# Performance work log

Hardware: AMD Instinct MI355X
Metric: run time of the kernel (lower is better)

The kernel has to match this reference:

```python
import jax, jax.numpy as jnp
import numpy as np
from jax import lax

C = 64; H = 128; W = 256; HW = H * W
HIDDEN = 64
D_STATE = 64; HEADDIM = 64; EXPAND = 2; CHUNK = 256; CONV_K = 4
D_INNER = EXPAND * C            # 128
NHEADS = D_INNER // HEADDIM     # 2
CONV_DIM = D_INNER + 2 * D_STATE  # 256
D_IN_PROJ = 2 * D_INNER + 2 * D_STATE + NHEADS  # 386
RECORD_LEN = [5, 3, 4, 2]
EPS = 1e-5


def setup_inputs() -> dict:
    key = jax.random.key(0)
    ks = jax.random.split(key, 16)
    def nrm(k, shape, scale=0.02):
        return scale * jax.random.normal(k, shape, jnp.float32)
    return {
        "xx": jax.random.normal(ks[0], (sum(RECORD_LEN), C, H, W), jnp.float32),
        "record_len": jnp.array(RECORD_LEN, jnp.int32),
        "score_w1": nrm(ks[1], (HIDDEN, C)),
        "score_b1": jnp.zeros((HIDDEN,), jnp.float32),
        "score_w2": nrm(ks[2], (1, HIDDEN)),
        "score_b2": jnp.zeros((1,), jnp.float32),
        "q_w": nrm(ks[3], (C, C)), "q_b": jnp.zeros((C,), jnp.float32),
        "k_w": nrm(ks[4], (C, C)), "k_b": jnp.zeros((C,), jnp.float32),
        "v_w": nrm(ks[5], (C, C)), "v_b": jnp.zeros((C,), jnp.float32),
        "ln_w": jnp.ones((C,), jnp.float32), "ln_b": jnp.zeros((C,), jnp.float32),
        "in_proj_w": nrm(ks[6], (D_IN_PROJ, C)),
        "in_proj_b": jnp.zeros((D_IN_PROJ,), jnp.float32),
        "conv_w": nrm(ks[7], (CONV_DIM, 1, CONV_K), 0.1),
        "conv_b": jnp.zeros((CONV_DIM,), jnp.float32),
        "dt_bias": 0.1 * jax.random.normal(ks[8], (NHEADS,), jnp.float32),
        "A_log": jnp.log(jnp.arange(1, NHEADS + 1, dtype=jnp.float32)),
        "ssd_D": jnp.ones((NHEADS,), jnp.float32),
        "rms_w": jnp.ones((D_INNER,), jnp.float32),
        "out_proj_w": nrm(ks[9], (C, D_INNER)),
    }


def _segsum(x):
    # x: (..., T) -> (..., T, T) with sum_{j<k<=i} x[k] below diagonal, -inf above
    T = x.shape[-1]
    cs = jnp.cumsum(x, -1)
    ss = cs[..., :, None] - cs[..., None, :]
    return jnp.where(jnp.tril(jnp.ones((T, T), bool)), ss, -jnp.inf)


def _ssd(x, A, Bm, Cm):
    # Mamba2 chunked SSD. x:(b,l,h,p) pre-scaled by dt; A:(b,l,h)=dt*A_head; Bm,Cm:(b,l,n) (ngroups=1)
    b, l, h, p = x.shape
    c = l // CHUNK
    x = x.reshape(b, c, CHUNK, h, p)
    A = A.reshape(b, c, CHUNK, h).transpose(0, 3, 1, 2)            # (b,h,c,cl)
    Bm = Bm.reshape(b, c, CHUNK, -1)
    Cm = Cm.reshape(b, c, CHUNK, -1)
    A_cum = jnp.cumsum(A, -1)
    Lmat = jnp.exp(_segsum(A))                                     # (b,h,c,cl,cl)
    Y_diag = jnp.einsum('bcln,bcsn,bhcls,bcshp->bclhp', Cm, Bm, Lmat, x)
    decay_states = jnp.exp(A_cum[..., -1:] - A_cum)                # (b,h,c,cl)
    states = jnp.einsum('bcln,bhcl,bclhp->bchpn', Bm, decay_states, x)
    padded = jnp.pad(A_cum[..., -1], ((0, 0), (0, 0), (1, 0)))     # (b,h,c+1)
    decay_chunk = jnp.exp(_segsum(padded))                         # (b,h,c+1,c+1)
    states_cat = jnp.concatenate([jnp.zeros_like(states[:, :1]), states], 1)
    states_in = jnp.einsum('bhzc,bchpn->bzhpn', decay_chunk, states_cat)[:, :-1]
    Y_off = jnp.einsum('bcln,bchpn,bhcl->bclhp', Cm, states_in, jnp.exp(A_cum))
    return (Y_diag + Y_off).reshape(b, l, h, p)


def _forward(xx, record_len, score_w1, score_b1, score_w2, score_b2,
             q_w, q_b, k_w, k_b, v_w, v_b, ln_w, ln_b,
             in_proj_w, in_proj_b, conv_w, conv_b,
             dt_bias, A_log, ssd_D, rms_w, out_proj_w):
    rl = [int(v) for v in np.asarray(record_len)]
    # score_mlp: 1x1 convs == per-pixel channel MLP, applied to all CAVs at once
    s = jax.nn.relu(jnp.einsum('nchw,dc->ndhw', xx, score_w1) + score_b1[None, :, None, None])
    scores = (jnp.einsum('ndhw,od->nohw', s, score_w2) + score_b2[None, :, None, None])[:, 0]  # (N,H,W)
    fused = []
    start = 0
    for n in rl:  # ragged groups (variable n_cav per sample)
        grp_sc = scores[start:start + n]
        idx = jnp.argmax(grp_sc, axis=0)  # topk k=1; softmax over singleton -> weight 1
        fused.append(jnp.take_along_axis(xx[start:start + n], idx[None, None], axis=0)[0])
        start += n
    fused = jnp.stack(fused)  # (B,C,H,W)
    Bsz = fused.shape[0]
    seq = fused.reshape(Bsz, C, HW).transpose(0, 2, 1)  # (B,L,C)
    # ScaledDotProductAttention on (HW,1,C): each position attends only to itself
    q = seq @ q_w.T + q_b
    k = seq @ k_w.T + k_b
    v = seq @ v_w.T + v_b
    score = jnp.sum(q * k, -1, keepdims=True) / np.float32(np.sqrt(C))  # (B,L,1)
    attn = jax.nn.softmax(score[..., None], axis=-1)[..., 0]            # == 1
    ctx = attn * v
    # VMAMBA2 block: pre-LayerNorm -> Mamba2 SSD -> residual
    mu = jnp.mean(ctx, -1, keepdims=True)
    var = jnp.var(ctx, -1, keepdims=True)
    u = (ctx - mu) / jnp.sqrt(var + EPS) * ln_w + ln_b
    zxbcdt = u @ in_proj_w.T + in_proj_b
    z = zxbcdt[..., :D_INNER]
    xBC = zxbcdt[..., D_INNER:D_INNER + CONV_DIM]
    dt = zxbcdt[..., D_INNER + CONV_DIM:]
    xBC = lax.conv_general_dilated(xBC.transpose(0, 2, 1), conv_w, (1,), [(CONV_K - 1, 0)],
                                   dimension_numbers=('NCH', 'OIH', 'NCH'),
                                   feature_group_count=CONV_DIM)
    xBC = jax.nn.silu(xBC + conv_b[None, :, None]).transpose(0, 2, 1)  # (B,L,CONV_DIM)
    xh = xBC[..., :D_INNER].reshape(Bsz, HW, NHEADS, HEADDIM)
    Bm = xBC[..., D_INNER:D_INNER + D_STATE]
    Cm = xBC[..., D_INNER + D_STATE:]
    dt = jax.nn.softplus(dt + dt_bias)  # (B,L,h)
    A = -jnp.exp(A_log)                 # (h,)
    y = _ssd(xh * dt[..., None], dt * A, Bm, Cm)
    y = y + ssd_D[None, None, :, None] * xh
    y = y.reshape(Bsz, HW, D_INNER)
    yz = y * jax.nn.silu(z)             # gated RMSNorm
    y = yz * lax.rsqrt(jnp.mean(yz * yz, -1, keepdims=True) + EPS) * rms_w
    h = ctx + y @ out_proj_w.T
    return h.transpose(0, 2, 1).reshape(Bsz, C, H, W)


def reference(xx, record_len, score_w1, score_b1, score_w2, score_b2,
              q_w, q_b, k_w, k_b, v_w, v_b, ln_w, ln_b,
              in_proj_w, in_proj_b, conv_w, conv_b,
              dt_bias, A_log, ssd_D, rms_w, out_proj_w):
    return _forward(xx, record_len, score_w1, score_b1, score_w2, score_b2,
                    q_w, q_b, k_w, k_b, v_w, v_b, ln_w, ln_b,
                    in_proj_w, in_proj_b, conv_w, conv_b,
                    dt_bias, A_log, ssd_D, rms_w, out_proj_w)
```

## Files before the change

### kernel.cpp

```cpp
#include <hip/hip_runtime.h>
#include <cmath>

#define HW 32768
#define NC 128
#define NH 2
#define B4 4

typedef __attribute__((ext_vector_type(8))) short bf16x8;
typedef __attribute__((ext_vector_type(4))) float f32x4;
typedef __attribute__((ext_vector_type(4))) ushort u16x4;
typedef __attribute__((ext_vector_type(8))) ushort u16x8;

__device__ __forceinline__ ushort f2b(float x) {
  union { float f; unsigned u; } v; v.f = x;
  unsigned r = v.u + 0x7FFFu + ((v.u >> 16) & 1u);
  return (ushort)(r >> 16);
}
__device__ __forceinline__ float b2f(ushort b) {
  union { unsigned u; float f; } v; v.u = ((unsigned)b) << 16;
  return v.f;
}
__device__ __forceinline__ int swz(int row, int k) { return k ^ ((row & 7) << 3); }
__device__ __forceinline__ bf16x8 ldfrag(const ushort* base, int row, int k, int stride) {
  return *(const bf16x8*)(base + row * stride + swz(row, k));
}

__global__ __launch_bounds__(256) void k_score_mfma(
    const float* __restrict__ xx, const float* __restrict__ w1,
    const float* __restrict__ b1, const float* __restrict__ w2,
    const float* __restrict__ b2, float* __restrict__ scores,
    int* __restrict__ cnt)
{
  __shared__ ushort Whi[64*64];
  __shared__ ushort Wlo[64*64];
  __shared__ ushort Xt[4][64*64];
  __shared__ float w2b1[128];
  int tid = threadIdx.x;
  if (blockIdx.x == 0 && tid == 0) cnt[0] = 0;
  for (int i = tid; i < 4096; i += 256) {
    int d = i >> 6, c = i & 63;
    float v = w1[i];
    ushort hi = f2b(v);
    int off = d*64 + swz(d, c);
    Whi[off] = hi;
    Wlo[off] = f2b(v - b2f(hi));
  }
  if (tid < 64) { w2b1[tid] = w2[tid]; w2b1[64+tid] = b1[tid]; }

  int wid = tid >> 6, lane = tid & 63;
  int n  = blockIdx.x >> 7;
  int t0 = (blockIdx.x & 127)*256 + wid*64;

  {
    const float* px = xx + (size_t)n*64*HW + t0 + lane;
    float xv[64];
    #pragma unroll
    for (int c = 0; c < 64; ++c) xv[c] = px[(size_t)c*HW];
    ushort* xh = Xt[wid];
    #pragma unroll
    for (int c8 = 0; c8 < 8; ++c8) {
      u16x8 p;
      #pragma unroll
      for (int j = 0; j < 8; ++j) p[j] = f2b(xv[c8*8 + j]);
      *(u16x8*)(xh + lane*64 + swz(lane, c8*8)) = p;
    }
  }
  __syncthreads();

  int lr = lane & 15, kb = lane >> 4;
  const ushort* xh = Xt[wid];
  f32x4 acc[4][4];
  #pragma unroll
  for (int m = 0; m < 4; ++m)
    #pragma unroll
    for (int nt = 0; nt < 4; ++nt) acc[m][nt] = (f32x4){0.f,0.f,0.f,0.f};
  #pragma unroll
  for (int k0 = 0; k0 < 64; k0 += 32) {
    bf16x8 ah[4], al[4], bx[4];
    #pragma unroll
    for (int m = 0; m < 4; ++m) {
      ah[m] = ldfrag(Whi, 16*m + lr, k0 + kb*8, 64);
      al[m] = ldfrag(Wlo, 16*m + lr, k0 + kb*8, 64);
    }
    #pragma unroll
    for (int nt = 0; nt < 4; ++nt) bx[nt] = ldfrag(xh, 16*nt + lr, k0 + kb*8, 64);
    #pragma unroll
    for (int m = 0; m < 4; ++m)
      #pragma unroll
      for (int nt = 0; nt < 4; ++nt) {
        acc[m][nt] = __builtin_amdgcn_mfma_f32_16x16x32_bf16(ah[m], bx[nt], acc[m][nt], 0, 0, 0);
        acc[m][nt] = __builtin_amdgcn_mfma_f32_16x16x32_bf16(al[m], bx[nt], acc[m][nt], 0, 0, 0);
      }
  }
  float bb2 = b2[0];
  #pragma unroll
  for (int nt = 0; nt < 4; ++nt) {
    float s = 0.f;
    #pragma unroll
    for (int m = 0; m < 4; ++m)
      #pragma unroll
      for (int r = 0; r < 4; ++r) {
        int d = 16*m + kb*4 + r;
        float h = acc[m][nt][r] + w2b1[64 + d];
        s += fmaxf(h, 0.f) * w2b1[d];
      }
    s += __shfl_xor(s, 16);
    s += __shfl_xor(s, 32);
    if (kb == 0) scores[(size_t)n*HW + t0 + 16*nt + lr] = s + bb2;
  }
}

__global__ __launch_bounds__(256) void k_argmax(
    const float* __restrict__ scores, int* __restrict__ idx,
    int* __restrict__ cnt, int* __restrict__ list)
{
  int i = blockIdx.x*256 + threadIdx.x;
  int g = i >> 15, t = i & (HW-1);
  const int gs0[4] = {0,5,8,12};
  const int gl0[4] = {5,3,4,2};
  int start = gs0[g], len = gl0[g];
  float best = scores[(size_t)start*HW + t];
  float second = -3.4e38f;
  int bi = start;
  for (int j = 1; j < len; ++j) {
    float s = scores[(size_t)(start+j)*HW + t];
    if (s > best) { second = best; best = s; bi = start + j; }
    else if (s > second) second = s;
  }
  idx[i] = bi;
  if (best - second < 5e-4f) {
    int p = atomicAdd(cnt, 1);
    list[p] = i;
  }
}

__global__ __launch_bounds__(256) void k_fix(
    const float* __restrict__ xx, const float* __restrict__ w1,
    const float* __restrict__ b1, const float* __restrict__ w2,
    const float* __restrict__ b2, const int* __restrict__ cnt,
    const int* __restrict__ list, int* __restrict__ idx)
{
  __shared__ float w1f[64*65];
  __shared__ float w2f[64], b1f[64];
  int tid = threadIdx.x;
  for (int i = tid; i < 4096; i += 256) w1f[(i >> 6)*65 + (i & 63)] = w1[i];
  if (tid < 64) { w2f[tid] = w2[tid]; b1f[tid] = b1[tid]; }
  __syncthreads();
  int n = cnt[0];
  int wid = tid >> 6, lane = tid & 63;
  int nwaves = gridDim.x * 4;
  const int gs0[4] = {0,5,8,12};
  const int gl0[4] = {5,3,4,2};
  double b2d = (double)b2[0];
  for (int e = blockIdx.x*4 + wid; e < n; e += nwaves) {
    int i = list[e];
    int g = i >> 15, t = i & (HW-1);
    int start = gs0[g], len = gl0[g];
    double best = -1e300;
    int bi = start;
    for (int j = 0; j < len; ++j) {
      double xv = (double)xx[(size_t)(start+j)*64*HW + (size_t)lane*HW + t];
      double acc = (double)b1f[lane];
      #pragma unroll
      for (int c = 0; c < 64; ++c) {
        double xc = __shfl(xv, c);
        acc += xc * (double)w1f[lane*65 + c];
      }
      double sc = (acc > 0.0 ? acc : 0.0) * (double)w2f[lane];
      #pragma unroll
      for (int m = 1; m < 64; m <<= 1) sc += __shfl_xor(sc, m);
      sc += b2d;
      if (sc > best) { best = sc; bi = start + j; }
    }
    if (lane == 0) idx[i] = bi;
  }
}

__global__ __launch_bounds__(256) void k_fuse(
    const float* __restrict__ xx, const int* __restrict__ idx,
    float* __restrict__ seq)
{
  __shared__ int idxs[64];
  __shared__ float tile[64*65];
  int tid = threadIdx.x;
  int g  = blockIdx.x >> 9;
  int t0 = (blockIdx.x & 511) << 6;
  if (tid < 64) idxs[tid] = idx[(size_t)g*HW + t0 + tid];
  __syncthreads();
  int tl = tid & 63, cq = tid >> 6;
  for (int r = 0; r < 16; ++r) {
    int c = r*4 + cq;
    tile[c*65 + tl] = xx[(size_t)idxs[tl]*64*HW + (size_t)c*HW + t0 + tl];
  }
  __syncthreads();
  for (int r = 0; r < 16; ++r) {
    int row = r*4 + cq;
    seq[((size_t)g*HW + t0 + row)*64 + tl] = tile[tl*65 + row];
  }
}

__global__ __launch_bounds__(256) void k_vln(
    const float* __restrict__ seq, const float* __restrict__ vw,
    const float* __restrict__ vb, const float* __restrict__ lnw,
    const float* __restrict__ lnb, float* __restrict__ ctx,
    ushort* __restrict__ usw)
{
  __shared__ float st[64*64];
  int tid = threadIdx.x;
  size_t p0 = (size_t)blockIdx.x * 64;
  for (int i = tid; i < 64*64; i += 256) st[i] = seq[p0*64 + i];
  int o = tid & 63, wv = tid >> 6;
  float w[64];
  const float4* w4 = (const float4*)(vw + o*64);
  #pragma unroll
  for (int c4 = 0; c4 < 16; ++c4) {
    float4 v = w4[c4];
    w[c4*4+0]=v.x; w[c4*4+1]=v.y; w[c4*4+2]=v.z; w[c4*4+3]=v.w;
  }
  float bias = vb[o], lw = lnw[o], lb = lnb[o];
  __syncthreads();
  const float4* st4 = (const float4*)st;
  for (int j = 0; j < 16; ++j) {
    int p = wv*16 + j;
    float acc = bias;
    #pragma unroll
    for (int c4 = 0; c4 < 16; ++c4) {
      float4 s4 = st4[p*16 + c4];
      acc += s4.x*w[c4*4] + s4.y*w[c4*4+1] + s4.z*w[c4*4+2] + s4.w*w[c4*4+3];
    }
    float s1 = acc, s2 = acc*acc;
    #pragma unroll
    for (int m = 1; m < 64; m <<= 1) {
      s1 += __shfl_xor(s1, m);
      s2 += __shfl_xor(s2, m);
    }
    float mu  = s1*(1.f/64.f);
    float var = s2*(1.f/64.f) - mu*mu;
    float rstd = rsqrtf(var + 1e-5f);
    size_t base = (p0+p)*64;
    int gt = (int)(p0 + p);
    ctx[base + o] = acc;
    usw[base + (o ^ (((gt+3)&7)<<3))] = f2b((acc - mu)*rstd*lw + lb);
  }
}

__global__ __launch_bounds__(256) void k_prep(
    const float* __restrict__ ipw, ushort* __restrict__ wsw)
{
  int i = blockIdx.x*256 + threadIdx.x;
  int row = i >> 6, c = i & 63;
  float v = (row < 386) ? ipw[row*64 + c] : 0.f;
  wsw[row*64 + swz(row, c)] = f2b(v);
}

__global__ __launch_bounds__(512) void k_gemm(
    const ushort* __restrict__ usw, const ushort* __restrict__ wsw,
    const float* __restrict__ ipb, const float* __restrict__ dtbias,
    ushort* __restrict__ z, ushort* __restrict__ xbcB, float* __restrict__ dt)
{
  __shared__ ushort Wlds[400*64];
  __shared__ ushort Ulds[80*64];
  __shared__ ushort trans[8704];
  int tid = threadIdx.x;
  int b  = blockIdx.x >> 9;
  int s  = blockIdx.x & 511;
  int t0 = s << 6;
  size_t pixbase = (size_t)b*HW + t0;
  size_t tilebase = ((size_t)(b*512 + s))*256*64;

  for (int i = tid; i < 3200; i += 512)
    *(u16x8*)(Wlds + i*8) = *(const u16x8*)(wsw + i*8);
  {
    const ushort* ubase = usw + ((size_t)b*HW + t0 - 3)*64;
    for (int i = tid; i < 536; i += 512) {
      u16x8 v;
      if (t0 == 0 && i < 24) v = (u16x8){0,0,0,0,0,0,0,0};
      else v = *(const u16x8*)(ubase + i*8);
      *(u16x8*)(Ulds + i*8) = v;
    }
  }
  __syncthreads();

  int w = tid >> 6, lane = tid & 63, lr = lane & 15, kb = lane >> 4;
  for (int rd = 0; rd < 3; ++rd) {
    int nt = rd*8 + w;
    f32x4 acc[5];
    #pragma unroll
    for (int mt = 0; mt < 5; ++mt) acc[mt] = (f32x4){0.f,0.f,0.f,0.f};
    #pragma unroll
    for (int kk = 0; kk < 64; kk += 32) {
      bf16x8 bfrag = ldfrag(Wlds, nt*16 + lr, kk + kb*8, 64);
      #pragma unroll
      for (int mt = 0; mt < 5; ++mt) {
        bf16x8 afrag = ldfrag(Ulds, mt*16 + lr, kk + kb*8, 64);
        acc[mt] = __builtin_amdgcn_mfma_f32_16x16x32_bf16(afrag, bfrag, acc[mt], 0, 0, 0);
      }
    }
    float bias = ipb[nt*16 + lr];
    if (rd == 0) {
      #pragma unroll
      for (int mt = 0; mt < 5; ++mt)
        #pragma unroll
        for (int r = 0; r < 4; ++r) {
          int t = mt*16 + kb*4 + r - 3;
          if (t >= 0 && t < 64) trans[t*132 + w*16 + lr] = f2b(acc[mt][r] + bias);
        }
    } else {
      #pragma unroll
      for (int mt = 0; mt < 5; ++mt)
        #pragma unroll
        for (int r = 0; r < 4; ++r) {
          int t = mt*16 + kb*4 + r - 3;
          if (t >= 0 && t < 64) trans[(w*16 + lr)*68 + t] = f2b(acc[mt][r] + bias);
        }
    }
    __syncthreads();
    if (rd == 0) {
      for (int i = tid; i < 2048; i += 512) {
        int t = i >> 5, c4 = (i & 31)*4;
        *(u16x4*)(z + (pixbase + t)*128 + c4) = *(const u16x4*)(trans + t*132 + c4);
      }
    } else {
      int chbase = (rd - 1)*128;
      for (int i = tid; i < 2048; i += 512) {
        int ch = i >> 4, t4 = (i & 15)*4;
        *(u16x4*)(xbcB + tilebase + (size_t)(chbase + ch)*64 + t4)
            = *(const u16x4*)(trans + ch*68 + t4);
      }
    }
    __syncthreads();
  }

  if (w == 0) {
    f32x4 acc[5];
    #pragma unroll
    for (int mt = 0; mt < 5; ++mt) acc[mt] = (f32x4){0.f,0.f,0.f,0.f};
    #pragma unroll
    for (int kk = 0; kk < 64; kk += 32) {
      bf16x8 bfrag = ldfrag(Wlds, 384 + lr, kk + kb*8, 64);
      #pragma unroll
      for (int mt = 0; mt < 5; ++mt) {
        bf16x8 afrag = ldfrag(Ulds, mt*16 + lr, kk + kb*8, 64);
        acc[mt] = __builtin_amdgcn_mfma_f32_16x16x32_bf16(afrag, bfrag, acc[mt], 0, 0, 0);
      }
    }
    if (lr < 2) {
      float bias = ipb[384 + lr] + dtbias[lr];
      #pragma unroll
      for (int mt = 0; mt < 5; ++mt)
        #pragma unroll
        for (int r = 0; r < 4; ++r) {
          int t = mt*16 + kb*4 + r - 3;
          if (t >= 0 && t < 64) {
            float a = acc[mt][r] + bias;
            dt[(pixbase + t)*2 + lr] = (a > 20.f) ? a : log1pf(expf(a));
          }
        }
    }
  }
}

__global__ __launch_bounds__(256) void k_conv(
    const ushort* __restrict__ xbcB, const float* __restrict__ convw,
    const float* __restrict__ convb, ushort* __restrict__ co2,
    ushort* __restrict__ Bm, ushort* __restrict__ Cm)
{
  __shared__ ushort bmc[64*132];
  int tid = threadIdx.x;
  int b  = blockIdx.x >> 9;
  int s  = blockIdx.x & 511;
  int lane = tid & 63, wv = tid >> 6;
  int toct = lane & 7, chi = lane >> 3;
  size_t tilebase = ((size_t)(b*512 + s))*256*64;
  const ushort* tsrc = xbcB + tilebase;
  const ushort* psrc = xbcB + tilebase - 256*64;

  for (int it = 0; it < 8; ++it) {
    int ch = wv*64 + it*8 + chi;
    u16x8 v = *(const u16x8*)(tsrc + ch*64 + toct*8);
    float x0 = b2f(v[0]), x1 = b2f(v[1]), x2 = b2f(v[2]), x3 = b2f(v[3]);
    float x4 = b2f(v[4]), x5 = b2f(v[5]), x6 = b2f(v[6]), x7 = b2f(v[7]);
    float pm1 = __shfl(x7, lane - 1);
    float pm2 = __shfl(x6, lane - 1);
    float pm3 = __shfl(x5, lane - 1);
    if (toct == 0) {
      if (s > 0) {
        u16x4 hq = *(const u16x4*)(psrc + ch*64 + 60);
        pm3 = b2f(hq[1]); pm2 = b2f(hq[2]); pm1 = b2f(hq[3]);
      } else {
        pm1 = pm2 = pm3 = 0.f;
      }
    }
    float4 cw = ((const float4*)convw)[ch];
    float cb = convb[ch];
    float o0 = cb + cw.x*pm3 + cw.y*pm2 + cw.z*pm1 + cw.w*x0;
    float o1 = cb + cw.x*pm2 + cw.y*pm1 + cw.z*x0  + cw.w*x1;
    float o2 = cb + cw.x*pm1 + cw.y*x0  + cw.z*x1  + cw.w*x2;
    float o3 = cb + cw.x*x0  + cw.y*x1  + cw.z*x2  + cw.w*x3;
    float o4 = cb + cw.x*x1  + cw.y*x2  + cw.z*x3  + cw.w*x4;
    float o5 = cb + cw.x*x2  + cw.y*x3  + cw.z*x4  + cw.w*x5;
    float o6 = cb + cw.x*x3  + cw.y*x4  + cw.z*x5  + cw.w*x6;
    float o7 = cb + cw.x*x4  + cw.y*x5  + cw.z*x6  + cw.w*x7;
    u16x8 ov;
    ov[0] = f2b(o0 / (1.f + __expf(-o0)));
    ov[1] = f2b(o1 / (1.f + __expf(-o1)));
    ov[2] = f2b(o2 / (1.f + __expf(-o2)));
    ov[3] = f2b(o3 / (1.f + __expf(-o3)));
    ov[4] = f2b(o4 / (1.f + __expf(-o4)));
    ov[5] = f2b(o5 / (1.f + __expf(-o5)));
    ov[6] = f2b(o6 / (1.f + __expf(-o6)));
    ov[7] = f2b(o7 / (1.f + __expf(-o7)));
    *(u16x8*)(co2 + tilebase + (size_t)ch*64 + toct*8) = ov;
    if (ch >= 128) {
      int c = ch - 128;
      int csw = c ^ (toct << 2);
      #pragma unroll
      for (int j = 0; j < 8; ++j)
        bmc[(toct*8 + j)*132 + csw] = ov[j];
    }
  }
  __syncthreads();
  size_t tg = (size_t)b*HW + s*64;
  for (int i = tid; i < 1024; i += 256) {
    int tt = i >> 4, n4 = (i & 15)*4;
    int sw = (tt >> 3) << 2;
    *(u16x4*)(Bm + (tg + tt)*64 + n4) = *(const u16x4*)(bmc + tt*132 + (n4 ^ sw));
    *(u16x4*)(Cm + (tg + tt)*64 + n4) = *(const u16x4*)(bmc + tt*132 + ((64 + n4) ^ sw));
  }
}

__global__ __launch_bounds__(256) void k_states(
    const float* __restrict__ dt, const ushort* __restrict__ co2,
    const float* __restrict__ A_log,
    float* __restrict__ states, float* __restrict__ A_last)
{
  extern __shared__ char smem[];
  float* ac  = (float*)smem;
  float* dec = ac + 256;
  ushort* xdT = (ushort*)(dec + 256);
  ushort* BT  = xdT + 16384;
  int tid = threadIdx.x;
  int ci = blockIdx.x, h = blockIdx.y, b = blockIdx.z;
  size_t tg = (size_t)b*HW + (size_t)ci*256;
  float Aneg = -expf(A_log[h]);
  float dv = dt[(tg + tid)*2 + h];
  ac[tid] = dv*Aneg;
  __syncthreads();
  for (int off = 1; off < 256; off <<= 1) {
    float v = (tid >= off) ? ac[tid - off] : 0.f;
    __syncthreads();
    ac[tid] += v;
    __syncthreads();
  }
  float alast = ac[255];
  dec[tid] = dv * __expf(alast - ac[tid]);
  __syncthreads();
  for (int i = tid; i < 64*32; i += 256) {
    int p = i >> 5, lc = (i & 31) * 8;
    int s = (ci << 2) + (lc >> 6);
    const ushort* cb2 = co2 + ((size_t)(b*512 + s))*256*64 + (lc & 63);
    u16x8 xv = *(const u16x8*)(cb2 + (size_t)(h*64 + p)*64);
    u16x8 o;
    #pragma unroll
    for (int e = 0; e < 8; ++e) o[e] = f2b(b2f(xv[e]) * dec[lc + e]);
    *(u16x8*)(xdT + p*256 + swz(p, lc)) = o;
    u16x8 bv = *(const u16x8*)(cb2 + (size_t)(128 + p)*64);
    *(u16x8*)(BT + p*256 + swz(p, lc)) = bv;
  }
  __syncthreads();
  int w = tid >> 6, lane = tid & 63, lr = lane & 15, kb = lane >> 4;
  f32x4 acc[4];
  #pragma unroll
  for (int m = 0; m < 4; ++m) acc[m] = (f32x4){0.f,0.f,0.f,0.f};
  for (int k0 = 0; k0 < 256; k0 += 32) {
    bf16x8 bfrag = ldfrag(BT, 16*w + lr, k0 + kb*8, 256);
    #pragma unroll
    for (int m = 0; m < 4; ++m) {
      bf16x8 afrag = ldfrag(xdT, 16*m + lr, k0 + kb*8, 256);
      acc[m] = __builtin_amdgcn_mfma_f32_16x16x32_bf16(afrag, bfrag, acc[m], 0, 0, 0);
    }
  }
  size_t sb = (((size_t)b*NC + ci)*NH + h)*4096;
  #pragma unroll
  for (int m = 0; m < 4; ++m)
    #pragma unroll
    for (int r = 0; r < 4; ++r)
      states[sb + (size_t)(16*m + kb*4 + r)*64 + 16*w + lr] = acc[m][r];
  if (tid == 0) A_last[((size_t)b*NH + h)*NC + ci] = alast;
}

__global__ __launch_bounds__(256) void k_scan(
    const float* __restrict__ states, const float* __restrict__ A_last,
    float* __restrict__ states_in)
{
  __shared__ float ef[NC];
  int tid = threadIdx.x;
  int seg = blockIdx.x & 7, h = (blockIdx.x >> 3) & 1, b = blockIdx.x >> 4;
  if (tid < NC) ef[tid] = __expf(A_last[((size_t)b*NH + h)*NC + tid]);
  __syncthreads();
  size_t base0 = (((size_t)b*NC)*NH + h)*4096 + seg*512 + tid;
  const size_t cstride = (size_t)NH*4096;
  float s0 = 0.f, s1 = 0.f;
  float ld0 = states[base0], ld1 = states[base0 + 256];
  for (int zc = 0; zc < NC; ++zc) {
    size_t cur = base0 + (size_t)zc*cstride;
    float n0 = 0.f, n1 = 0.f;
    if (zc < NC-1) { n0 = states[cur + cstride]; n1 = states[cur + cstride + 256]; }
    states_in[cur] = s0; states_in[cur + 256] = s1;
    float e = ef[zc];
    s0 = ld0 + e*s0; s1 = ld1 + e*s1;
    ld0 = n0; ld1 = n1;
  }
}

__global__ __launch_bounds__(512) void k_ydiag(
    const float* __restrict__ dt, const ushort* __restrict__ co2,
    const ushort* __restrict__ Bm, const ushort* __restrict__ Cm,
    const float* __restrict__ states_in, const float* __restrict__ A_log,
    const float* __restrict__ ssd_D, ushort* __restrict__ y)
{
  extern __shared__ char smem[];
  float* ac   = (float*)smem;
  float* dts  = ac + 256;
  float* segs = dts + 256;
  ushort* Cb  = (ushort*)(segs + 8);
  ushort* Bb  = Cb + 16384;
  ushort* xsT = Bb + 16384;
  ushort* Sb  = xsT + 16384;
  ushort* Wb  = Sb + 4096;
  int tid = threadIdx.x;
  int ci = blockIdx.x, h = blockIdx.y, b = blockIdx.z;
  size_t tg = (size_t)b*HW + (size_t)ci*256;
  int w = tid >> 6, lane = tid & 63, lr = lane & 15, kb = lane >> 4;
  float Aneg = -expf(A_log[h]);

  float dv = 0.f, a = 0.f;
  if (tid < 256) {
    dv = dt[(tg + tid)*2 + h];
    a = dv*Aneg;
    #pragma unroll
    for (int d = 1; d < 64; d <<= 1) {
      float t = __shfl_up(a, d);
      if (lane >= d) a += t;
    }
    if (lane == 63) segs[w] = a;
  }
  __syncthreads();
  if (tid < 256) {
    float off = 0.f;
    #pragma unroll
    for (int j = 0; j < 4; ++j) if (j < w) off += segs[j];
    ac[tid] = a + off;
    dts[tid] = dv;
  }

  for (int i = tid; i < 256*16; i += 512) {
    int l = i >> 4, n4 = (i & 15) * 4;
    u16x4 cv = *(const u16x4*)(Cm + (tg + l)*64 + n4);
    *(u16x4*)(Cb + l*64 + swz(l, n4)) = cv;
    u16x4 bv = *(const u16x4*)(Bm + (tg + l)*64 + n4);
    *(u16x4*)(Bb + l*64 + swz(l, n4)) = bv;
  }
  {
    const ushort* ct0 = co2 + ((size_t)(b*512 + (ci << 2)))*16384 + (size_t)h*4096;
    for (int i = tid; i < 64*32; i += 512) {
      int p = i >> 5, sc = (i & 31) * 8;
      u16x8 xv = *(const u16x8*)(ct0 + (size_t)(sc >> 6)*16384 + (size_t)p*64 + (sc & 63));
      *(u16x8*)(xsT + p*256 + swz(p, sc)) = xv;
    }
  }
  size_t sbg = (((size_t)b*NC + ci)*NH + h)*4096;
  for (int i = tid; i < 1024; i += 512) {
    int p = i >> 4, n4 = (i & 15) * 4;
    float4 sv = *(const float4*)(states_in + sbg + p*64 + n4);
    u16x4 pk = { f2b(sv.x), f2b(sv.y), f2b(sv.z), f2b(sv.w) };
    *(u16x4*)(Sb + p*64 + swz(p, n4)) = pk;
  }
  __syncthreads();

  int l0 = w*32;
  ushort* Ww = Wb + w*2304;

  f32x4 yy[2][4];
  #pragma unroll
  for (int m = 0; m < 2; ++m)
    #pragma unroll
    for (int n = 0; n < 4; ++n) yy[m][n] = (f32x4){0.f,0.f,0.f,0.f};
  #pragma unroll
  for (int kk = 0; kk < 64; kk += 32) {
    bf16x8 af[2], bf[4];
    #pragma unroll
    for (int m = 0; m < 2; ++m) af[m] = ldfrag(Cb, l0 + 16*m + lr, kk + kb*8, 64);
    #pragma unroll
    for (int n = 0; n < 4; ++n) bf[n] = ldfrag(Sb, 16*n + lr, kk + kb*8, 64);
    #pragma unroll
    for (int m = 0; m < 2; ++m)
      #pragma unroll
      for (int n = 0; n < 4; ++n)
        yy[m][n] = __builtin_amdgcn_mfma_f32_16x16x32_bf16(af[m], bf[n], yy[m][n], 0, 0, 0);
  }
  #pragma unroll
  for (int m = 0; m < 2; ++m)
    #pragma unroll
    for (int r = 0; r < 4; ++r) {
      float e = __expf(ac[l0 + 16*m + kb*4 + r]);
      #pragma unroll
      for (int n = 0; n < 4; ++n) yy[m][n][r] *= e;
    }

  int nst = (w >> 1) + 1;
  for (int st = 0; st < nst; ++st) {
    int s0 = st*64;
    f32x4 g[2][4];
    #pragma unroll
    for (int m = 0; m < 2; ++m)
      #pragma unroll
      for (int n = 0; n < 4; ++n) g[m][n] = (f32x4){0.f,0.f,0.f,0.f};
    #pragma unroll
    for (int kk = 0; kk < 64; kk += 32) {
      bf16x8 af[2], bf[4];
      #pragma unroll
      for (int m = 0; m < 2; ++m) af[m] = ldfrag(Cb, l0 + 16*m + lr, kk + kb*8, 64);
      #pragma unroll
      for (int n = 0; n < 4; ++n) bf[n] = ldfrag(Bb, s0 + 16*n + lr, kk + kb*8, 64);
      #pragma unroll
      for (int m = 0; m < 2; ++m)
        #pragma unroll
        for (int n = 0; n < 4; ++n)
          g[m][n] = __builtin_amdgcn_mfma_f32_16x16x32_bf16(af[m], bf[n], g[m][n], 0, 0, 0);
    }
    #pragma unroll
    for (int m = 0; m < 2; ++m)
      #pragma unroll
      for (int r = 0; r < 4; ++r) {
        int lrow = 16*m + kb*4 + r;
        int lg = l0 + lrow;
        float acl = ac[lg];
        #pragma unroll
        for (int n = 0; n < 4; ++n) {
          int sl = 16*n + lr;
          int sg = s0 + sl;
          float v = (sg <= lg) ? g[m][n][r] * __expf(acl - ac[sg]) * dts[sg] : 0.f;
          Ww[lrow*72 + sl] = f2b(v);
        }
      }
    #pragma unroll
    for (int kk = 0; kk < 64; kk += 32) {
      bf16x8 af[2], bf[4];
      #pragma unroll
      for (int m = 0; m < 2; ++m)
        af[m] = *(const bf16x8*)(Ww + (16*m + lr)*72 + kk + kb*8);
      #pragma unroll
      for (int n = 0; n < 4; ++n) bf[n] = ldfrag(xsT, 16*n + lr, s0 + kk + kb*8, 256);
      #pragma unroll
      for (int m = 0; m < 2; ++m)
        #pragma unroll
        for (int n = 0; n < 4; ++n)
          yy[m][n] = __builtin_amdgcn_mfma_f32_16x16x32_bf16(af[m], bf[n], yy[m][n], 0, 0, 0);
    }
  }

  float Dh = ssd_D[h];
  #pragma unroll
  for (int m = 0; m < 2; ++m)
    #pragma unroll
    for (int r = 0; r < 4; ++r) {
      int lg = l0 + 16*m + kb*4 + r;
      #pragma unroll
      for (int n = 0; n < 4; ++n) {
        int p = 16*n + lr;
        float val = yy[m][n][r] + Dh * b2f(xsT[p*256 + swz(p, lg)]);
        y[(tg + lg)*128 + h*64 + p] = f2b(val);
      }
    }
}

__global__ __launch_bounds__(256) void k_final(
    const ushort* __restrict__ y, const ushort* __restrict__ z,
    const float* __restrict__ ctx, const float* __restrict__ rms_w,
    const float* __restrict__ opw, float* __restrict__ out)
{
  __shared__ ushort yn[64*128];
  __shared__ ushort wop[64*128];
  __shared__ float otile[64*65];
  int tid = threadIdx.x;
  size_t p0 = (size_t)blockIdx.x * 64;

  for (int i = tid; i < 2048; i += 256) {
    int row = i >> 5, c4 = (i & 31) * 4;
    float4 v = ((const float4*)(opw + row*128))[c4 >> 2];
    float4 rw = ((const float4*)rms_w)[c4 >> 2];
    u16x4 p = { f2b(v.x*rw.x), f2b(v.y*rw.y), f2b(v.z*rw.z), f2b(v.w*rw.w) };
    *(u16x4*)(wop + row*128 + swz(row, c4)) = p;
  }

  {
    int t = tid >> 2, q = tid & 3;
    const u16x4* yp = (const u16x4*)(y + (p0 + t)*128 + q*32);
    const u16x4* zp = (const u16x4*)(z + (p0 + t)*128 + q*32);
    float vals[32];
    float ss = 0.f;
    #pragma unroll
    for (int j = 0; j < 8; ++j) {
      u16x4 yv = yp[j];
      u16x4 zv = zp[j];
      #pragma unroll
      for (int e = 0; e < 4; ++e) {
        float zf = b2f(zv[e]);
        float x = b2f(yv[e]) * (zf / (1.f + __expf(-zf)));
        vals[j*4+e] = x; ss += x*x;
      }
    }
    ss += __shfl_xor(ss, 1);
    ss += __shfl_xor(ss, 2);
    float rinv = rsqrtf(ss*(1.f/128.f) + 1e-5f);
    #pragma unroll
    for (int j = 0; j < 8; ++j) {
      int c4 = q*32 + j*4;
      u16x4 p = { f2b(vals[j*4]*rinv), f2b(vals[j*4+1]*rinv),
                  f2b(vals[j*4+2]*rinv), f2b(vals[j*4+3]*rinv) };
      *(u16x4*)(yn + t*128 + swz(t, c4)) = p;
    }
  }
  __syncthreads();

  int w = tid >> 6, lane = tid & 63, lr = lane & 15, kb = lane >> 4;
  f32x4 acc[4];
  #pragma unroll
  for (int n = 0; n < 4; ++n) acc[n] = (f32x4){0.f,0.f,0.f,0.f};
  #pragma unroll
  for (int kk = 0; kk < 128; kk += 32) {
    bf16x8 a = ldfrag(yn, w*16 + lr, kk + kb*8, 128);
    #pragma unroll
    for (int n = 0; n < 4; ++n) {
      bf16x8 bf = ldfrag(wop, n*16 + lr, kk + kb*8, 128);
      acc[n] = __builtin_amdgcn_mfma_f32_16x16x32_bf16(a, bf, acc[n], 0, 0, 0);
    }
  }
  #pragma unroll
  for (int n = 0; n < 4; ++n)
    #pragma unroll
    for (int r = 0; r < 4; ++r) {
      int tok = w*16 + kb*4 + r, ch = n*16 + lr;
      otile[ch*65 + tok] = acc[n][r] + ctx[(p0 + tok)*64 + ch];
    }
  __syncthreads();
  {
    size_t b  = p0 >> 15;
    size_t t0 = p0 & (HW-1);
    for (int r = 0; r < 16; ++r) {
      int cc = r*4 + (tid >> 6);
      int pp = tid & 63;
      out[(b*64 + cc)*HW + t0 + pp] = otile[cc*65 + pp];
    }
  }
}

extern "C" void kernel_launch(void* const* d_in, const int* in_sizes, int n_in,
                              void* d_out, int out_size, void* d_ws, size_t ws_size,
                              hipStream_t stream) {
  (void)in_sizes; (void)n_in; (void)out_size; (void)ws_size;
  const float* xx   = (const float*)d_in[0];
  const float* sw1  = (const float*)d_in[2];
  const float* sb1  = (const float*)d_in[3];
  const float* sw2  = (const float*)d_in[4];
  const float* sb2  = (const float*)d_in[5];
  const float* vw   = (const float*)d_in[10];
  const float* vb   = (const float*)d_in[11];
  const float* lnw  = (const float*)d_in[12];
  const float* lnb  = (const float*)d_in[13];
  const float* ipw  = (const float*)d_in[14];
  const float* ipb  = (const float*)d_in[15];
  const float* cw   = (const float*)d_in[16];
  const float* cb   = (const float*)d_in[17];
  const float* dtb  = (const float*)d_in[18];
  const float* alog = (const float*)d_in[19];
  const float* sd   = (const float*)d_in[20];
  const float* rmsw = (const float*)d_in[21];
  const float* opw  = (const float*)d_in[22];

  float* ws = (float*)d_ws;
  float*  scores32 = ws;
  int*    idxb     = (int*)(ws + 458752);
  int*    cntb     = (int*)(ws + 589824);
  int*    listb    = (int*)(ws + 589832);
  float*  dtp      = ws;
  float*  seq      = ws + 917504;
  ushort* Cmb      = (ushort*)(ws + 917504);
  ushort* Bmb      = (ushort*)(ws + 5111808);
  float*  ctx      = ws + 9306112;
  ushort* uswb     = (ushort*)(ws + 17694720);
  float*  states   = ws + 17694720;
  float*  states_in= ws + 21889024;
  ushort* zb       = (ushort*)(ws + 26083328);
  ushort* xbcBb    = (ushort*)(ws + 34471936);
  ushort* co2b     = (ushort*)(ws + 51249152);
  ushort* yb       = (ushort*)(ws + 68026368);
  float*  Alast    = ws + 84803584;
  ushort* wswb     = (ushort*)(ws + 84804608);

  k_score_mfma<<<1792, 256, 0, stream>>>(xx, sw1, sb1, sw2, sb2, scores32, cntb);
  k_argmax<<<512, 256, 0, stream>>>(scores32, idxb, cntb, listb);
  k_fix<<<512, 256, 0, stream>>>(xx, sw1, sb1, sw2, sb2, cntb, listb, idxb);
  k_fuse<<<2048, 256, 0, stream>>>(xx, idxb, seq);
  k_vln<<<2048, 256, 0, stream>>>(seq, vw, vb, lnw, lnb, ctx, uswb);
  k_prep<<<100, 256, 0, stream>>>(ipw, wswb);
  k_gemm<<<2048, 512, 0, stream>>>(uswb, wswb, ipb, dtb, zb, xbcBb, dtp);
  k_conv<<<2048, 256, 0, stream>>>(xbcBb, cw, cb, co2b, Bmb, Cmb);
  dim3 gssd(NC, NH, B4);
  k_states<<<gssd, 256, 67584, stream>>>(dtp, co2b, alog, states, Alast);
  k_scan<<<64, 256, 0, stream>>>(states, Alast, states_in);
  k_ydiag<<<gssd, 512, 145440, stream>>>(dtp, co2b, Bmb, Cmb, states_in, alog, sd, yb);
  k_final<<<2048, 256, 0, stream>>>(yb, zb, ctx, rmsw, opw, (float*)d_out);
}
```

Baseline: 415.7 us.

## Amortize gemm weight loads over four tiles; balance ydiag causal strips across waves

The in_proj GEMM kernel now processes four 64-pixel tiles per block. The 50KB weight tile is loaded into LDS once per block instead of once per tile, and the grid shrinks from 2048 to 512 blocks. The ydiag kernel assigns each wave a pair of 16-row strips (w and 15-w), so the triangular intra-chunk work is spread evenly across waves and the per-wave scratch and dynamic LDS shrink. The tradeoffs are fewer blocks to hide latency in the GEMM, plus extra serialization from the per-tile loop and its barriers.

```diff
diff --git a/kernel.cpp b/kernel.cpp
--- a/kernel.cpp
+++ b/kernel.cpp
@@ -262,101 +262,106 @@
   __shared__ ushort Ulds[80*64];
   __shared__ ushort trans[8704];
   int tid = threadIdx.x;
-  int b  = blockIdx.x >> 9;
-  int s  = blockIdx.x & 511;
-  int t0 = s << 6;
-  size_t pixbase = (size_t)b*HW + t0;
-  size_t tilebase = ((size_t)(b*512 + s))*256*64;
+  int b     = blockIdx.x >> 7;
+  int chunk = blockIdx.x & 127;
+  int w = tid >> 6, lane = tid & 63, lr = lane & 15, kb = lane >> 4;
 
   for (int i = tid; i < 3200; i += 512)
     *(u16x8*)(Wlds + i*8) = *(const u16x8*)(wsw + i*8);
-  {
-    const ushort* ubase = usw + ((size_t)b*HW + t0 - 3)*64;
-    for (int i = tid; i < 536; i += 512) {
-      u16x8 v;
-      if (t0 == 0 && i < 24) v = (u16x8){0,0,0,0,0,0,0,0};
-      else v = *(const u16x8*)(ubase + i*8);
-      *(u16x8*)(Ulds + i*8) = v;
-    }
-  }
-  __syncthreads();
-
-  int w = tid >> 6, lane = tid & 63, lr = lane & 15, kb = lane >> 4;
-  for (int rd = 0; rd < 3; ++rd) {
-    int nt = rd*8 + w;
-    f32x4 acc[5];
-    #pragma unroll
-    for (int mt = 0; mt < 5; ++mt) acc[mt] = (f32x4){0.f,0.f,0.f,0.f};
-    #pragma unroll
-    for (int kk = 0; kk < 64; kk += 32) {
-      bf16x8 bfrag = ldfrag(Wlds, nt*16 + lr, kk + kb*8, 64);
-      #pragma unroll
-      for (int mt = 0; mt < 5; ++mt) {
-        bf16x8 afrag = ldfrag(Ulds, mt*16 + lr, kk + kb*8, 64);
-        acc[mt] = __builtin_amdgcn_mfma_f32_16x16x32_bf16(afrag, bfrag, acc[mt], 0, 0, 0);
-      }
-    }
-    float bias = ipb[nt*16 + lr];
-    if (rd == 0) {
-      #pragma unroll
-      for (int mt = 0; mt < 5; ++mt)
-        #pragma unroll
-        for (int r = 0; r < 4; ++r) {
-          int t = mt*16 + kb*4 + r - 3;
-          if (t >= 0 && t < 64) trans[t*132 + w*16 + lr] = f2b(acc[mt][r] + bias);
+
+  for (int it = 0; it < 4; ++it) {
+    int s = chunk*4 + it;
+    int t0 = s << 6;
+    size_t pixbase = (size_t)b*HW + t0;
+    size_t tilebase = ((size_t)(b*512 + s))*256*64;
+    {
+      const ushort* ubase = usw + ((size_t)b*HW + t0 - 3)*64;
+      for (int i = tid; i < 536; i += 512) {
+        u16x8 v;
+        if (t0 == 0 && i < 24) v = (u16x8){0,0,0,0,0,0,0,0};
+        else v = *(const u16x8*)(ubase + i*8);
+        *(u16x8*)(Ulds + i*8) = v;
+      }
+    }
+    __syncthreads();
+
+    for (int rd = 0; rd < 3; ++rd) {
+      int nt = rd*8 + w;
+      f32x4 acc[5];
+      #pragma unroll
+      for (int mt = 0; mt < 5; ++mt) acc[mt] = (f32x4){0.f,0.f,0.f,0.f};
+      #pragma unroll
+      for (int kk = 0; kk < 64; kk += 32) {
+        bf16x8 bfrag = ldfrag(Wlds, nt*16 + lr, kk + kb*8, 64);
+        #pragma unroll
+        for (int mt = 0; mt < 5; ++mt) {
+          bf16x8 afrag = ldfrag(Ulds, mt*16 + lr, kk + kb*8, 64);
+          acc[mt] = __builtin_amdgcn_mfma_f32_16x16x32_bf16(afrag, bfrag, acc[mt], 0, 0, 0);
         }
-    } else {
-      #pragma unroll
-      for (int mt = 0; mt < 5; ++mt)
-        #pragma unroll
-        for (int r = 0; r < 4; ++r) {
-          int t = mt*16 + kb*4 + r - 3;
-          if (t >= 0 && t < 64) trans[(w*16 + lr)*68 + t] = f2b(acc[mt][r] + bias);
+      }
+      float bias = ipb[nt*16 + lr];
+      if (rd == 0) {
+        #pragma unroll
+        for (int mt = 0; mt < 5; ++mt)
+          #pragma unroll
+          for (int r = 0; r < 4; ++r) {
+            int t = mt*16 + kb*4 + r - 3;
+            if (t >= 0 && t < 64) trans[t*132 + w*16 + lr] = f2b(acc[mt][r] + bias);
+          }
+      } else {
+        #pragma unroll
+        for (int mt = 0; mt < 5; ++mt)
+          #pragma unroll
+          for (int r = 0; r < 4; ++r) {
+            int t = mt*16 + kb*4 + r - 3;
+            if (t >= 0 && t < 64) trans[(w*16 + lr)*68 + t] = f2b(acc[mt][r] + bias);
+          }
+      }
+      __syncthreads();
+      if (rd == 0) {
+        for (int i = tid; i < 2048; i += 512) {
+          int t = i >> 5, c4 = (i & 31)*4;
+          *(u16x4*)(z + (pixbase + t)*128 + c4) = *(const u16x4*)(trans + t*132 + c4);
         }
+      } else {
+        int chbase = (rd - 1)*128;
+        for (int i = tid; i < 2048; i += 512) {
+          int ch = i >> 4, t4 = (i & 15)*4;
+          *(u16x4*)(xbcB + tilebase + (size_t)(chbase + ch)*64 + t4)
+              = *(const u16x4*)(trans + ch*68 + t4);
+        }
+      }
+      __syncthreads();
+    }
+
+    if (w == 0) {
+      f32x4 acc[5];
+      #pragma unroll
+      for (int mt = 0; mt < 5; ++mt) acc[mt] = (f32x4){0.f,0.f,0.f,0.f};
+      #pragma unroll
+      for (int kk = 0; kk < 64; kk += 32) {
+        bf16x8 bfrag = ldfrag(Wlds, 384 + lr, kk + kb*8, 64);
+        #pragma unroll
+        for (int mt = 0; mt < 5; ++mt) {
+          bf16x8 afrag = ldfrag(Ulds, mt*16 + lr, kk + kb*8, 64);
+          acc[mt] = __builtin_amdgcn_mfma_f32_16x16x32_bf16(afrag, bfrag, acc[mt], 0, 0, 0);
+        }
+      }
+      if (lr < 2) {
+        float bias = ipb[384 + lr] + dtbias[lr];
+        #pragma unroll
+        for (int mt = 0; mt < 5; ++mt)
+          #pragma unroll
+          for (int r = 0; r < 4; ++r) {
+            int t = mt*16 + kb*4 + r - 3;
+            if (t >= 0 && t < 64) {
+              float a = acc[mt][r] + bias;
+              dt[(pixbase + t)*2 + lr] = (a > 20.f) ? a : log1pf(expf(a));
+            }
+          }
+      }
     }
     __syncthreads();
-    if (rd == 0) {
-      for (int i = tid; i < 2048; i += 512) {
-        int t = i >> 5, c4 = (i & 31)*4;
-        *(u16x4*)(z + (pixbase + t)*128 + c4) = *(const u16x4*)(trans + t*132 + c4);
-      }
-    } else {
-      int chbase = (rd - 1)*128;
-      for (int i = tid; i < 2048; i += 512) {
-        int ch = i >> 4, t4 = (i & 15)*4;
-        *(u16x4*)(xbcB + tilebase + (size_t)(chbase + ch)*64 + t4)
-            = *(const u16x4*)(trans + ch*68 + t4);
-      }
-    }
-    __syncthreads();
-  }
-
-  if (w == 0) {
-    f32x4 acc[5];
-    #pragma unroll
-    for (int mt = 0; mt < 5; ++mt) acc[mt] = (f32x4){0.f,0.f,0.f,0.f};
-    #pragma unroll
-    for (int kk = 0; kk < 64; kk += 32) {
-      bf16x8 bfrag = ldfrag(Wlds, 384 + lr, kk + kb*8, 64);
-      #pragma unroll
-      for (int mt = 0; mt < 5; ++mt) {
-        bf16x8 afrag = ldfrag(Ulds, mt*16 + lr, kk + kb*8, 64);
-        acc[mt] = __builtin_amdgcn_mfma_f32_16x16x32_bf16(afrag, bfrag, acc[mt], 0, 0, 0);
-      }
-    }
-    if (lr < 2) {
-      float bias = ipb[384 + lr] + dtbias[lr];
-      #pragma unroll
-      for (int mt = 0; mt < 5; ++mt)
-        #pragma unroll
-        for (int r = 0; r < 4; ++r) {
-          int t = mt*16 + kb*4 + r - 3;
-          if (t >= 0 && t < 64) {
-            float a = acc[mt][r] + bias;
-            dt[(pixbase + t)*2 + lr] = (a > 20.f) ? a : log1pf(expf(a));
-          }
-        }
-    }
   }
 }
 
@@ -578,98 +583,92 @@
   }
   __syncthreads();
 
-  int l0 = w*32;
-  ushort* Ww = Wb + w*2304;
+  int strips[2] = { w, 15 - w };
+  ushort* Ww = Wb + w*1152;
 
   f32x4 yy[2][4];
   #pragma unroll
-  for (int m = 0; m < 2; ++m)
-    #pragma unroll
-    for (int n = 0; n < 4; ++n) yy[m][n] = (f32x4){0.f,0.f,0.f,0.f};
+  for (int sp = 0; sp < 2; ++sp)
+    #pragma unroll
+    for (int n = 0; n < 4; ++n) yy[sp][n] = (f32x4){0.f,0.f,0.f,0.f};
   #pragma unroll
   for (int kk = 0; kk < 64; kk += 32) {
     bf16x8 af[2], bf[4];
     #pragma unroll
-    for (int m = 0; m < 2; ++m) af[m] = ldfrag(Cb, l0 + 16*m + lr, kk + kb*8, 64);
+    for (int sp = 0; sp < 2; ++sp) af[sp] = ldfrag(Cb, strips[sp]*16 + lr, kk + kb*8, 64);
     #pragma unroll
     for (int n = 0; n < 4; ++n) bf[n] = ldfrag(Sb, 16*n + lr, kk + kb*8, 64);
     #pragma unroll
-    for (int m = 0; m < 2; ++m)
+    for (int sp = 0; sp < 2; ++sp)
       #pragma unroll
       for (int n = 0; n < 4; ++n)
-        yy[m][n] = __builtin_amdgcn_mfma_f32_16x16x32_bf16(af[m], bf[n], yy[m][n], 0, 0, 0);
-  }
-  #pragma unroll
-  for (int m = 0; m < 2; ++m)
+        yy[sp][n] = __builtin_amdgcn_mfma_f32_16x16x32_bf16(af[sp], bf[n], yy[sp][n], 0, 0, 0);
+  }
+  #pragma unroll
+  for (int sp = 0; sp < 2; ++sp)
     #pragma unroll
     for (int r = 0; r < 4; ++r) {
-      float e = __expf(ac[l0 + 16*m + kb*4 + r]);
-      #pragma unroll
-      for (int n = 0; n < 4; ++n) yy[m][n][r] *= e;
-    }
-
-  int nst = (w >> 1) + 1;
-  for (int st = 0; st < nst; ++st) {
-    int s0 = st*64;
-    f32x4 g[2][4];
-    #pragma unroll
-    for (int m = 0; m < 2; ++m)
-      #pragma unroll
-      for (int n = 0; n < 4; ++n) g[m][n] = (f32x4){0.f,0.f,0.f,0.f};
-    #pragma unroll
-    for (int kk = 0; kk < 64; kk += 32) {
-      bf16x8 af[2], bf[4];
-      #pragma unroll
-      for (int m = 0; m < 2; ++m) af[m] = ldfrag(Cb, l0 + 16*m + lr, kk + kb*8, 64);
-      #pragma unroll
-      for (int n = 0; n < 4; ++n) bf[n] = ldfrag(Bb, s0 + 16*n + lr, kk + kb*8, 64);
-      #pragma unroll
-      for (int m = 0; m < 2; ++m)
+      float e = __expf(ac[strips[sp]*16 + kb*4 + r]);
+      #pragma unroll
+      for (int n = 0; n < 4; ++n) yy[sp][n][r] *= e;
+    }
+
+  #pragma unroll
+  for (int sp = 0; sp < 2; ++sp) {
+    int strip = strips[sp];
+    int l0 = strip*16;
+    int nst = (strip >> 2) + 1;
+    for (int st = 0; st < nst; ++st) {
+      int s0 = st*64;
+      f32x4 g[4];
+      #pragma unroll
+      for (int n = 0; n < 4; ++n) g[n] = (f32x4){0.f,0.f,0.f,0.f};
+      #pragma unroll
+      for (int kk = 0; kk < 64; kk += 32) {
+        bf16x8 af = ldfrag(Cb, l0 + lr, kk + kb*8, 64);
+        bf16x8 bf[4];
+        #pragma unroll
+        for (int n = 0; n < 4; ++n) bf[n] = ldfrag(Bb, s0 + 16*n + lr, kk + kb*8, 64);
         #pragma unroll
         for (int n = 0; n < 4; ++n)
-          g[m][n] = __builtin_amdgcn_mfma_f32_16x16x32_bf16(af[m], bf[n], g[m][n], 0, 0, 0);
-    }
-    #pragma unroll
-    for (int m = 0; m < 2; ++m)
+          g[n] = __builtin_amdgcn_mfma_f32_16x16x32_bf16(af, bf[n], g[n], 0, 0, 0);
+      }
       #pragma unroll
       for (int r = 0; r < 4; ++r) {
-        int lrow = 16*m + kb*4 + r;
+        int lrow = kb*4 + r;
         int lg = l0 + lrow;
         float acl = ac[lg];
         #pragma unroll
         for (int n = 0; n < 4; ++n) {
           int sl = 16*n + lr;
           int sg = s0 + sl;
-          float v = (sg <= lg) ? g[m][n][r] * __expf(acl - ac[sg]) * dts[sg] : 0.f;
+          float v = (sg <= lg) ? g[n][r] * __expf(acl - ac[sg]) * dts[sg] : 0.f;
           Ww[lrow*72 + sl] = f2b(v);
         }
       }
-    #pragma unroll
-    for (int kk = 0; kk < 64; kk += 32) {
-      bf16x8 af[2], bf[4];
-      #pragma unroll
-      for (int m = 0; m < 2; ++m)
-        af[m] = *(const bf16x8*)(Ww + (16*m + lr)*72 + kk + kb*8);
-      #pragma unroll
-      for (int n = 0; n < 4; ++n) bf[n] = ldfrag(xsT, 16*n + lr, s0 + kk + kb*8, 256);
-      #pragma unroll
-      for (int m = 0; m < 2; ++m)
+      #pragma unroll
+      for (int kk = 0; kk < 64; kk += 32) {
+        bf16x8 af = *(const bf16x8*)(Ww + lr*72 + kk + kb*8);
+        bf16x8 bf[4];
+        #pragma unroll
+        for (int n = 0; n < 4; ++n) bf[n] = ldfrag(xsT, 16*n + lr, s0 + kk + kb*8, 256);
         #pragma unroll
         for (int n = 0; n < 4; ++n)
-          yy[m][n] = __builtin_amdgcn_mfma_f32_16x16x32_bf16(af[m], bf[n], yy[m][n], 0, 0, 0);
+          yy[sp][n] = __builtin_amdgcn_mfma_f32_16x16x32_bf16(af, bf[n], yy[sp][n], 0, 0, 0);
+      }
     }
   }
 
   float Dh = ssd_D[h];
   #pragma unroll
-  for (int m = 0; m < 2; ++m)
+  for (int sp = 0; sp < 2; ++sp)
     #pragma unroll
     for (int r = 0; r < 4; ++r) {
-      int lg = l0 + 16*m + kb*4 + r;
+      int lg = strips[sp]*16 + kb*4 + r;
       #pragma unroll
       for (int n = 0; n < 4; ++n) {
         int p = 16*n + lr;
-        float val = yy[m][n][r] + Dh * b2f(xsT[p*256 + swz(p, lg)]);
+        float val = yy[sp][n][r] + Dh * b2f(xsT[p*256 + swz(p, lg)]);
         y[(tg + lg)*128 + h*64 + p] = f2b(val);
       }
     }
@@ -805,11 +804,11 @@
   k_fuse<<<2048, 256, 0, stream>>>(xx, idxb, seq);
   k_vln<<<2048, 256, 0, stream>>>(seq, vw, vb, lnw, lnb, ctx, uswb);
   k_prep<<<100, 256, 0, stream>>>(ipw, wswb);
-  k_gemm<<<2048, 512, 0, stream>>>(uswb, wswb, ipb, dtb, zb, xbcBb, dtp);
+  k_gemm<<<512, 512, 0, stream>>>(uswb, wswb, ipb, dtb, zb, xbcBb, dtp);
   k_conv<<<2048, 256, 0, stream>>>(xbcBb, cw, cb, co2b, Bmb, Cmb);
   dim3 gssd(NC, NH, B4);
   k_states<<<gssd, 256, 67584, stream>>>(dtp, co2b, alog, states, Alast);
   k_scan<<<64, 256, 0, stream>>>(states, Alast, states_in);
-  k_ydiag<<<gssd, 512, 145440, stream>>>(dtp, co2b, Bmb, Cmb, states_in, alog, sd, yb);
+  k_ydiag<<<gssd, 512, 127008, stream>>>(dtp, co2b, Bmb, Cmb, states_in, alog, sd, yb);
   k_final<<<2048, 256, 0, stream>>>(yb, zb, ctx, rmsw, opw, (float*)d_out);
 }
```

Result: faster. 397.2 us (-4.5%).
